# Optimization experiments

Measured on AMD Instinct MI355X. Metric: run time of the kernel, lower is better.

## Reference

```python
import jax, jax.numpy as jnp
import numpy as np

GROUP_SIZE = 64
NUM_HEADS = 16
NUM_KV_HEADS = 4
ROPE_BASE = 10000.0


def rms_norm(x):
    eps = jnp.asarray(jnp.finfo(x.dtype).eps, x.dtype)
    return x * jax.lax.rsqrt(jnp.mean(x * x, axis=-1, keepdims=True) + eps)


def ternary_weight(w, g=GROUP_SIZE):
    # fake-quant with straight-through estimator, matching torch bf16 cast
    wb = w.astype(jnp.bfloat16)
    wg = wb.reshape(-1, g)
    scale = jnp.clip(jnp.mean(jnp.abs(wg), axis=-1, keepdims=True), 1e-8)
    q = jnp.clip(jnp.round(wg / scale), -1, 1)
    wq = (q * scale).reshape(w.shape)
    return wb + jax.lax.stop_gradient(wq - wb)


def ternary_linear(x, w):
    wt = ternary_weight(w).astype(x.dtype)
    return x @ wt.T


def apply_rotary_emb(x, cos, sin):
    half = x.shape[-1] // 2
    x1, x2 = x[..., :half], x[..., half:]
    return jnp.concatenate((x1 * cos + x2 * sin, x1 * -sin + x2 * cos), axis=-1)


def rotary_tables(seq_len, head_dim, dtype):
    inv_freq = 1.0 / (ROPE_BASE ** (jnp.arange(0, head_dim, 2, dtype=jnp.float32) / head_dim))
    freqs = jnp.outer(jnp.arange(seq_len, dtype=jnp.float32), inv_freq)  # [S, D/2]
    cos = jnp.cos(freqs)[None, :, None, :].astype(dtype)  # [1,S,1,D/2]
    sin = jnp.sin(freqs)[None, :, None, :].astype(dtype)
    return cos, sin


def setup_inputs() -> dict:
    key = jax.random.key(0)
    k1, k2, k3 = jax.random.split(key, 3)
    dim = 1024
    q_size = NUM_HEADS * (dim // NUM_HEADS)
    kv_size = NUM_KV_HEADS * (dim // NUM_HEADS)
    return {
        "x": jax.random.normal(k1, (2, 2048, dim), dtype=jnp.float32),
        "w_qkv": jax.random.normal(k2, (q_size + 2 * kv_size, dim), dtype=jnp.float32) * 0.02,
        "w_proj": jax.random.normal(k3, (dim, dim), dtype=jnp.float32) * 0.02,
        "q_gain": jnp.ones((NUM_HEADS,), dtype=jnp.float32),
    }


def reference(x, w_qkv, w_proj, q_gain):
    bsz, seqlen, dim = x.shape
    head_dim = dim // NUM_HEADS
    q_size = NUM_HEADS * head_dim
    kv_size = NUM_KV_HEADS * head_dim

    qkv = ternary_linear(x, w_qkv)
    q = qkv[..., :q_size].reshape(bsz, seqlen, NUM_HEADS, head_dim)
    k = qkv[..., q_size:q_size + kv_size].reshape(bsz, seqlen, NUM_KV_HEADS, head_dim)
    v = qkv[..., q_size + kv_size:].reshape(bsz, seqlen, NUM_KV_HEADS, head_dim)

    q, k = rms_norm(q), rms_norm(k)
    cos, sin = rotary_tables(seqlen, head_dim, q.dtype)
    q = apply_rotary_emb(q, cos, sin)
    k = apply_rotary_emb(k, cos, sin)
    q = q * q_gain.astype(q.dtype)[None, None, :, None]

    # GQA: repeat kv heads
    rep = NUM_HEADS // NUM_KV_HEADS
    kr = jnp.repeat(k, rep, axis=2)  # [B,S,H,D]
    vr = jnp.repeat(v, rep, axis=2)

    scale = 1.0 / jnp.sqrt(jnp.asarray(head_dim, q.dtype))
    scores = jnp.einsum('bqhd,bkhd->bhqk', q, kr) * scale  # [B,H,S,S]
    causal = jnp.tril(jnp.ones((seqlen, seqlen), dtype=bool))
    scores = jnp.where(causal[None, None], scores, jnp.asarray(-jnp.inf, scores.dtype))
    probs = jax.nn.softmax(scores, axis=-1)
    y = jnp.einsum('bhqk,bkhd->bqhd', probs, vr).reshape(bsz, seqlen, dim)

    # NormedTernaryLinear: rms_norm then ternary linear
    return ternary_linear(rms_norm(y), w_proj)
```

## Files before the change

kernel.cpp:

```cpp
#include <hip/hip_runtime.h>
#include <cstdint>

typedef unsigned short u16;
typedef __bf16 bf16x8 __attribute__((ext_vector_type(8)));
typedef short s16x4 __attribute__((ext_vector_type(4)));
typedef int s32x2 __attribute__((ext_vector_type(2)));
typedef float f32x4 __attribute__((ext_vector_type(4)));

__device__ __forceinline__ u16 f2bf(float f) {
    unsigned u = __float_as_uint(f);
    u = (u + 0x7fffu + ((u >> 16) & 1u)) >> 16;
    return (u16)u;
}
__device__ __forceinline__ float bf2f(u16 h) {
    return __uint_as_float(((unsigned)h) << 16);
}

__device__ __forceinline__ void glds16(const u16* g, u16* l) {
    __builtin_amdgcn_global_load_lds(
        (const __attribute__((address_space(1))) void*)g,
        (__attribute__((address_space(3))) void*)l, 16, 0, 0);
}

__device__ __forceinline__ s16x4 pack_bf4(float p0, float p1, float p2, float p3) {
    unsigned a0 = __float_as_uint(p0) + 0x8000u;
    unsigned a1 = __float_as_uint(p1) + 0x8000u;
    unsigned a2 = __float_as_uint(p2) + 0x8000u;
    unsigned a3 = __float_as_uint(p3) + 0x8000u;
    s32x2 pk = {(int)__builtin_amdgcn_perm(a1, a0, 0x07060302u),
                (int)__builtin_amdgcn_perm(a3, a2, 0x07060302u)};
    return __builtin_bit_cast(s16x4, pk);
}

#if __has_builtin(__builtin_amdgcn_mfma_f32_16x16x16bf16_1k)
#define MFMA16(a, b, c) __builtin_amdgcn_mfma_f32_16x16x16bf16_1k(a, b, c, 0, 0, 0)
#else
static __device__ __forceinline__ f32x4 mfma16_asm(s16x4 a, s16x4 b, f32x4 c) {
    asm("v_mfma_f32_16x16x16_bf16 %0, %1, %2, %0" : "+v"(c) : "v"(a), "v"(b));
    return c;
}
#define MFMA16(a, b, c) mfma16_asm(a, b, c)
#endif

__global__ __launch_bounds__(256) void prep(
    const float* __restrict__ w_qkv, const float* __restrict__ w_proj,
    const float* __restrict__ x,
    u16* __restrict__ wqkv_b, u16* __restrict__ wproj_b, u16* __restrict__ xb) {
    int bid = blockIdx.x;
    if (bid < 1280) {
        const float* w; u16* o; size_t base;
        if (bid < 768) { w = w_qkv; o = wqkv_b; base = (size_t)bid * 2048; }
        else { w = w_proj; o = wproj_b; base = (size_t)(bid - 768) * 2048; }
        size_t i = base + (size_t)threadIdx.x * 8;
        float4 A = *(const float4*)(w + i);
        float4 B = *(const float4*)(w + i + 4);
        float wf[8] = {A.x, A.y, A.z, A.w, B.x, B.y, B.z, B.w};
        float wbf[8], ab[8];
        #pragma unroll
        for (int e = 0; e < 8; ++e) { wbf[e] = bf2f(f2bf(wf[e])); ab[e] = fabsf(wbf[e]); }
        float s = ((ab[0] + ab[1]) + (ab[2] + ab[3])) + ((ab[4] + ab[5]) + (ab[6] + ab[7]));
        s += __shfl_xor(s, 1);
        s += __shfl_xor(s, 2);
        s += __shfl_xor(s, 4);
        float scale = bf2f(f2bf(s * (1.0f / 64.0f)));
        if (scale < 1e-8f) scale = 1e-8f;
        u16 ov[8];
        #pragma unroll
        for (int e = 0; e < 8; ++e) {
            float t = bf2f(f2bf(wbf[e] / scale));
            float q = rintf(t);
            q = fminf(1.0f, fmaxf(-1.0f, q));
            float d = bf2f(f2bf(q * scale - wbf[e]));
            ov[e] = f2bf(wbf[e] + d);
        }
        *(int4*)(o + i) = *(const int4*)ov;
    } else {
        size_t i = ((size_t)(bid - 1280) * 256 + threadIdx.x) * 8;
        float4 a = *(const float4*)(x + i);
        float4 b = *(const float4*)(x + i + 4);
        u16 o[8] = {f2bf(a.x), f2bf(a.y), f2bf(a.z), f2bf(a.w),
                    f2bf(b.x), f2bf(b.y), f2bf(b.z), f2bf(b.w)};
        *(int4*)(xb + i) = *(const int4*)o;
    }
}

__global__ __launch_bounds__(256) void gemm_qkv(
    const u16* __restrict__ A, const u16* __restrict__ B,
    const float* __restrict__ gain,
    u16* __restrict__ Qb, u16* __restrict__ Kb, u16* __restrict__ Vt) {
    __shared__ u16 As[2][256 * 32];
    __shared__ u16 Bs[2][64 * 32];
    const int tid = threadIdx.x;
    const int lane = tid & 63, w = tid >> 6;
    const int quad = lane >> 4, l16 = lane & 15;
    const int bx = blockIdx.x, by = blockIdx.y;
    const int n0 = bx * 64, t0 = by * 256;
    const bool vblk = bx >= 20;
    const int K = 1024, nk = 32;
    const int b = by >> 3;

    const int sra = w * 16 + (lane >> 2);
    const int srb = tid >> 2;
    const int sg4 = lane & 3;

    f32x4 acc[4][4];
    f32x4 zero = {0.f, 0.f, 0.f, 0.f};
    #pragma unroll
    for (int i = 0; i < 4; ++i)
        #pragma unroll
        for (int j = 0; j < 4; ++j) acc[i][j] = zero;

    int aoff[4], boff[4];
    #pragma unroll
    for (int mi = 0; mi < 4; ++mi) {
        int r = w * 64 + mi * 16 + l16;
        aoff[mi] = r * 32 + (quad ^ ((r >> 1) & 3)) * 8;
    }
    #pragma unroll
    for (int ni = 0; ni < 4; ++ni) {
        int rb = ni * 16 + l16;
        boff[ni] = rb * 32 + (quad ^ ((rb >> 1) & 3)) * 8;
    }

    #pragma unroll
    for (int i = 0; i < 4; ++i) {
        int r = sra + i * 64;
        int g = sg4 ^ ((r >> 1) & 3);
        glds16(A + (size_t)(t0 + r) * K + g * 8, &As[0][0] + (w * 16 + i * 64) * 32 + lane * 8);
    }
    {
        int g = sg4 ^ ((srb >> 1) & 3);
        glds16(B + (size_t)(n0 + srb) * K + g * 8, &Bs[0][0] + w * 512 + lane * 8);
    }
    __syncthreads();

    for (int kt = 0; kt < nk; ++kt) {
        if (kt + 1 < nk) {
            int k0 = (kt + 1) * 32, bi = (kt + 1) & 1;
            #pragma unroll
            for (int i = 0; i < 4; ++i) {
                int r = sra + i * 64;
                int g = sg4 ^ ((r >> 1) & 3);
                glds16(A + (size_t)(t0 + r) * K + k0 + g * 8, &As[bi][0] + (w * 16 + i * 64) * 32 + lane * 8);
            }
            int g = sg4 ^ ((srb >> 1) & 3);
            glds16(B + (size_t)(n0 + srb) * K + k0 + g * 8, &Bs[bi][0] + w * 512 + lane * 8);
        }
        const u16* as = &As[kt & 1][0];
        const u16* bs = &Bs[kt & 1][0];
        bf16x8 af[4], bfr[4];
        #pragma unroll
        for (int mi = 0; mi < 4; ++mi) af[mi]  = *(const bf16x8*)(as + aoff[mi]);
        #pragma unroll
        for (int ni = 0; ni < 4; ++ni) bfr[ni] = *(const bf16x8*)(bs + boff[ni]);
        if (!vblk) {
            #pragma unroll
            for (int mi = 0; mi < 4; ++mi)
                #pragma unroll
                for (int ni = 0; ni < 4; ++ni)
                    acc[mi][ni] = __builtin_amdgcn_mfma_f32_16x16x32_bf16(af[mi], bfr[ni], acc[mi][ni], 0, 0, 0);
        } else {
            #pragma unroll
            for (int mi = 0; mi < 4; ++mi)
                #pragma unroll
                for (int ni = 0; ni < 4; ++ni)
                    acc[mi][ni] = __builtin_amdgcn_mfma_f32_16x16x32_bf16(bfr[ni], af[mi], acc[mi][ni], 0, 0, 0);
        }
        __syncthreads();
    }

    if (vblk) {
        const int kv = bx - 20;
        u16* vbase = Vt + (size_t)(b * 4 + kv) * 64 * 2048;
        const int si = (t0 + w * 64 + l16) & 2047;
        #pragma unroll
        for (int mi = 0; mi < 4; ++mi)
            #pragma unroll
            for (int ni = 0; ni < 4; ++ni) {
                int d = ni * 16 + quad * 4;
                #pragma unroll
                for (int r = 0; r < 4; ++r)
                    vbase[(size_t)(d + r) * 2048 + si + mi * 16] = f2bf(acc[mi][ni][r]);
            }
    } else {
        const bool isQ = bx < 16;
        const float sc = 0.18033688011112042f;
        const float g = isQ ? gain[bx] * sc : 1.0f;
        u16* base = isQ ? (Qb + (size_t)(b * 16 + bx) * 2048 * 64)
                        : (Kb + (size_t)(b * 4 + (bx - 16)) * 2048 * 64);
        const float eps = 1.1920929e-7f;
        const float invf0 = (float)(1.0 / pow(10000.0, (double)l16 / 32.0));
        const float invf1 = (float)(1.0 / pow(10000.0, (double)(l16 + 16) / 32.0));
        #pragma unroll
        for (int mi = 0; mi < 4; ++mi) {
            #pragma unroll
            for (int r = 0; r < 4; ++r) {
                float v0 = acc[mi][0][r], v1 = acc[mi][1][r];
                float v2 = acc[mi][2][r], v3 = acc[mi][3][r];
                float ssq = (v0 * v0 + v1 * v1) + (v2 * v2 + v3 * v3);
                #pragma unroll
                for (int m = 1; m < 16; m <<= 1) ssq += __shfl_xor(ssq, m);
                float rn = 1.0f / sqrtf(ssq * (1.0f / 64.0f) + eps);
                int si = (t0 + w * 64 + mi * 16 + quad * 4 + r) & 2047;
                float a0 = (float)si * invf0, a1 = (float)si * invf1;
                float c0 = __cosf(a0), s0 = __sinf(a0);
                float c1 = __cosf(a1), s1 = __sinf(a1);
                float x1a = v0 * rn, x2a = v2 * rn;
                float x1b = v1 * rn, x2b = v3 * rn;
                u16* row = base + (size_t)si * 64;
                row[l16]      = f2bf((x1a * c0 + x2a * s0) * g);
                row[l16 + 32] = f2bf((x2a * c0 - x1a * s0) * g);
                row[l16 + 16] = f2bf((x1b * c1 + x2b * s1) * g);
                row[l16 + 48] = f2bf((x2b * c1 - x1b * s1) * g);
            }
        }
    }
}

__global__ __launch_bounds__(256) void gemm_bt(
    const u16* __restrict__ A, const u16* __restrict__ B,
    float* __restrict__ C, int M, int N, int K) {
    __shared__ u16 As[2][128 * 32];
    __shared__ u16 Bs[2][64 * 32];
    const int tid = threadIdx.x;
    const int lane = tid & 63, w = tid >> 6;
    const int quad = lane >> 4, l16 = lane & 15;
    const int m0 = blockIdx.y * 128, n0 = blockIdx.x * 64;
    const int wm = (w >> 1) * 64, wn = (w & 1) * 32;

    const int sra = w * 16 + (lane >> 2);
    const int srb = tid >> 2;
    const int sg4 = lane & 3;

    f32x4 acc[4][2];
    f32x4 zero = {0.f, 0.f, 0.f, 0.f};
    #pragma unroll
    for (int i = 0; i < 4; ++i) { acc[i][0] = zero; acc[i][1] = zero; }

    int aoff[4], boff[2];
    #pragma unroll
    for (int mi = 0; mi < 4; ++mi) {
        int r = wm + mi * 16 + l16;
        aoff[mi] = r * 32 + (quad ^ ((r >> 1) & 3)) * 8;
    }
    #pragma unroll
    for (int ni = 0; ni < 2; ++ni) {
        int r = wn + ni * 16 + l16;
        boff[ni] = r * 32 + (quad ^ ((r >> 1) & 3)) * 8;
    }

    const int nk = K >> 5;
    #pragma unroll
    for (int i = 0; i < 2; ++i) {
        int r = sra + i * 64;
        int g = sg4 ^ ((r >> 1) & 3);
        glds16(A + (size_t)(m0 + r) * K + g * 8, &As[0][0] + (w * 16 + i * 64) * 32 + lane * 8);
    }
    {
        int g = sg4 ^ ((srb >> 1) & 3);
        glds16(B + (size_t)(n0 + srb) * K + g * 8, &Bs[0][0] + w * 512 + lane * 8);
    }
    __syncthreads();

    for (int kt = 0; kt < nk; ++kt) {
        if (kt + 1 < nk) {
            int k0 = (kt + 1) * 32, bi = (kt + 1) & 1;
            #pragma unroll
            for (int i = 0; i < 2; ++i) {
                int r = sra + i * 64;
                int g = sg4 ^ ((r >> 1) & 3);
                glds16(A + (size_t)(m0 + r) * K + k0 + g * 8, &As[bi][0] + (w * 16 + i * 64) * 32 + lane * 8);
            }
            int g = sg4 ^ ((srb >> 1) & 3);
            glds16(B + (size_t)(n0 + srb) * K + k0 + g * 8, &Bs[bi][0] + w * 512 + lane * 8);
        }
        const u16* as = &As[kt & 1][0];
        const u16* bs = &Bs[kt & 1][0];
        bf16x8 af[4], bfr[2];
        #pragma unroll
        for (int mi = 0; mi < 4; ++mi) af[mi]  = *(const bf16x8*)(as + aoff[mi]);
        #pragma unroll
        for (int ni = 0; ni < 2; ++ni) bfr[ni] = *(const bf16x8*)(bs + boff[ni]);
        #pragma unroll
        for (int mi = 0; mi < 4; ++mi)
            #pragma unroll
            for (int ni = 0; ni < 2; ++ni)
                acc[mi][ni] = __builtin_amdgcn_mfma_f32_16x16x32_bf16(af[mi], bfr[ni], acc[mi][ni], 0, 0, 0);
        __syncthreads();
    }
    #pragma unroll
    for (int mi = 0; mi < 4; ++mi)
        #pragma unroll
        for (int ni = 0; ni < 2; ++ni) {
            int rg = m0 + wm + mi * 16 + quad * 4;
            int cg = n0 + wn + ni * 16 + l16;
            float* cp = C + (size_t)rg * N + cg;
            #pragma unroll
            for (int r = 0; r < 4; ++r) cp[(size_t)r * N] = acc[mi][ni][r];
        }
}

__global__ __launch_bounds__(512, 4) void attn(
    const u16* __restrict__ Qb, const u16* __restrict__ Kb,
    const u16* __restrict__ Vt, const float* __restrict__ gain,
    float* __restrict__ y, float* __restrict__ Opart, float* __restrict__ ml) {
    __shared__ u16 Ks[2][64 * 64];
    __shared__ u16 Vsh[2][64 * 64];
    const int hb = blockIdx.x;
    const int h = hb & 15, b = hb >> 4, kvh = h >> 2;
    const int yid = blockIdx.y;
    int bq, c0; bool partial;
    if (yid < 16) { bq = 15 - (yid >> 1); c0 = (yid & 1) * 16; partial = true; }
    else          { bq = 23 - yid;        c0 = 0;              partial = false; }
    const int nj = partial ? (c0 ? (2 * bq - 14) : 16) : (2 * bq + 2);
    const int q0 = bq * 128;
    const int tid = threadIdx.x, lane = tid & 63, w = tid >> 6;
    const int quad = lane >> 4, l16 = lane & 15;
    const float nM = -(12.0f * fabsf(gain[h]) + 1.0f);

    const u16* Qg = Qb + ((size_t)(b * 16 + h) * 2048 + q0) * 64;
    const u16* Kg = Kb + (size_t)(b * 4 + kvh) * 2048 * 64;
    const u16* Vg = Vt + (size_t)(b * 4 + kvh) * 64 * 2048;

    const bf16x8 qa0 = *(const bf16x8*)(Qg + (size_t)(w * 16 + l16) * 64 + quad * 8);
    const bf16x8 qa1 = *(const bf16x8*)(Qg + (size_t)(w * 16 + l16) * 64 + 32 + quad * 8);

    const int sr = tid >> 3;
    const int sg = (tid & 7) ^ (sr & 7);
    u16* kd[2] = {&Ks[0][0] + tid * 8, &Ks[1][0] + tid * 8};
    u16* vd[2] = {&Vsh[0][0] + tid * 8, &Vsh[1][0] + tid * 8};

    {
        int c = (c0 + nj - 1) * 64;
        glds16(Kg + (size_t)(c + sr) * 64 + sg * 8, kd[(nj - 1) & 1]);
        glds16(Vg + (size_t)sr * 2048 + c + sg * 8, vd[(nj - 1) & 1]);
    }
    __syncthreads();

    f32x4 o[4];
    f32x4 zero = {0.f, 0.f, 0.f, 0.f};
    #pragma unroll
    for (int t = 0; t < 4; ++t) o[t] = zero;
    float l = 0.f;

    for (int jj = nj - 1; jj >= 0; --jj) {
        if (jj > 0) {
            int c = (c0 + jj - 1) * 64;
            glds16(Kg + (size_t)(c + sr) * 64 + sg * 8, kd[(jj - 1) & 1]);
            glds16(Vg + (size_t)sr * 2048 + c + sg * 8, vd[(jj - 1) & 1]);
        }
        const u16* Kt = (jj & 1) ? &Ks[1][0] : &Ks[0][0];
        const u16* Vl = (jj & 1) ? &Vsh[1][0] : &Vsh[0][0];
        const int d = 8 * bq + w - 4 * (c0 + jj);
        if (d >= 0) {
            const int tmax = d < 3 ? d : 3;
            f32x4 st[4];
            #pragma unroll
            for (int t = 0; t < 4; ++t) {
                if (t <= tmax) {
                    int rk = t * 16 + l16;
                    bf16x8 kb0 = *(const bf16x8*)(Kt + rk * 64 + ((quad ^ (rk & 7)) * 8));
                    bf16x8 kb1 = *(const bf16x8*)(Kt + rk * 64 + (((quad + 4) ^ (rk & 7)) * 8));
                    f32x4 s = __builtin_amdgcn_mfma_f32_16x16x32_bf16(kb0, qa0, zero, 0, 0, 0);
                    s = __builtin_amdgcn_mfma_f32_16x16x32_bf16(kb1, qa1, s, 0, 0, 0);
                    if (t == d) {
                        #pragma unroll
                        for (int r = 0; r < 4; ++r)
                            if (quad * 4 + r > l16) s[r] = -1e30f;
                    }
                    st[t] = s;
                }
            }
            float rs = 0.f;
            s16x4 pf[4];
            #pragma unroll
            for (int t = 0; t < 4; ++t) {
                if (t <= tmax) {
                    float p0 = __builtin_amdgcn_exp2f(st[t][0] + nM);
                    float p1 = __builtin_amdgcn_exp2f(st[t][1] + nM);
                    float p2 = __builtin_amdgcn_exp2f(st[t][2] + nM);
                    float p3 = __builtin_amdgcn_exp2f(st[t][3] + nM);
                    rs += (p0 + p1) + (p2 + p3);
                    pf[t] = pack_bf4(p0, p1, p2, p3);
                }
            }
            rs += __shfl_xor(rs, 16);
            rs += __shfl_xor(rs, 32);
            l += rs;
            #pragma unroll
            for (int dt = 0; dt < 4; ++dt) {
                int rv = dt * 16 + l16;
                #pragma unroll
                for (int kt = 0; kt < 4; ++kt) {
                    if (kt <= tmax) {
                        int gv = 2 * kt + (quad >> 1);
                        s16x4 va = *(const s16x4*)(Vl + rv * 64 + ((gv ^ (rv & 7)) * 8) + (quad & 1) * 4);
                        o[dt] = MFMA16(va, pf[kt], o[dt]);
                    }
                }
            }
        }
        __syncthreads();
    }

    const int q = w * 16 + l16;
    if (!partial) {
        const float inv = 1.0f / l;
        const size_t row = (size_t)b * 2048 + q0 + q;
        #pragma unroll
        for (int dt = 0; dt < 4; ++dt) {
            f32x4 a = o[dt] * inv;
            *(f32x4*)(&y[row * 1024 + h * 64 + dt * 16 + quad * 4]) = a;
        }
    } else {
        const int slot = (hb * 8 + (bq - 8)) * 2 + (c0 ? 1 : 0);
        float* Op = Opart + (size_t)slot * 8192;
        #pragma unroll
        for (int dt = 0; dt < 4; ++dt)
            *(f32x4*)(Op + q * 64 + dt * 16 + quad * 4) = o[dt];
        if (quad == 0) ml[slot * 128 + q] = l;
    }
}

__global__ __launch_bounds__(256) void rmsnorm_merge(
    const float* __restrict__ y, const float* __restrict__ Opart,
    const float* __restrict__ ml, u16* __restrict__ yb) {
    __shared__ float red[4];
    const int row = blockIdx.x, tid = threadIdx.x;
    const int b = row >> 11, s = row & 2047;
    float4 v;
    if (s < 1024) {
        v = *(const float4*)(y + (size_t)row * 1024 + tid * 4);
    } else {
        const int bq = s >> 7, q = s & 127;
        const int e = tid * 4, h = e >> 6, dh = e & 63;
        const int slot = ((b * 16 + h) * 8 + (bq - 8)) * 2;
        float l0 = ml[slot * 128 + q];
        float l1 = ml[(slot + 1) * 128 + q];
        float inv = 1.0f / (l0 + l1);
        const float* P0 = Opart + (size_t)slot * 8192 + q * 64 + dh;
        f32x4 x0 = *(const f32x4*)P0;
        f32x4 x1 = *(const f32x4*)(P0 + 8192);
        f32x4 r = (x0 + x1) * inv;
        v.x = r[0]; v.y = r[1]; v.z = r[2]; v.w = r[3];
    }
    float ss = v.x * v.x + v.y * v.y + v.z * v.z + v.w * v.w;
    #pragma unroll
    for (int m = 1; m < 64; m <<= 1) ss += __shfl_xor(ss, m);
    if ((tid & 63) == 0) red[tid >> 6] = ss;
    __syncthreads();
    float tot = red[0] + red[1] + red[2] + red[3];
    float rn = 1.0f / sqrtf(tot * (1.0f / 1024.0f) + 1.1920929e-7f);
    u16 o[4] = {f2bf(v.x * rn), f2bf(v.y * rn), f2bf(v.z * rn), f2bf(v.w * rn)};
    *(uint2*)(yb + (size_t)row * 1024 + tid * 4) = *(const uint2*)o;
}

extern "C" void kernel_launch(void* const* d_in, const int* in_sizes, int n_in,
                              void* d_out, int out_size, void* d_ws, size_t ws_size,
                              hipStream_t stream) {
    const float* x      = (const float*)d_in[0];
    const float* w_qkv  = (const float*)d_in[1];
    const float* w_proj = (const float*)d_in[2];
    const float* q_gain = (const float*)d_in[3];
    float* out = (float*)d_out;
    char* ws = (char*)d_ws;

    u16*   wproj_b = (u16*)(ws);
    u16*   xb      = (u16*)(ws + 2097152);
    float* y       = (float*)(ws + 2097152);
    u16*   wqkv_b  = (u16*)(ws + 10485760);
    u16*   Qb      = (u16*)(ws + 18874368);
    u16*   yb      = (u16*)(ws + 18874368);
    u16*   Kb      = (u16*)(ws + 27262976);
    u16*   Vt      = (u16*)(ws + 29360128);
    float* Opart   = (float*)(ws + 31457280);
    float* mlb     = (float*)(ws + 48234496);

    prep<<<3328, 256, 0, stream>>>(w_qkv, w_proj, x, wqkv_b, wproj_b, xb);
    gemm_qkv<<<dim3(24, 16), 256, 0, stream>>>(xb, wqkv_b, q_gain, Qb, Kb, Vt);
    attn<<<dim3(32, 24), 512, 0, stream>>>(Qb, Kb, Vt, q_gain, y, Opart, mlb);
    rmsnorm_merge<<<4096, 256, 0, stream>>>(y, Opart, mlb, yb);
    gemm_bt<<<dim3(16, 32), 256, 0, stream>>>(yb, wproj_b, out, 4096, 1024, 1024);
}
```

Baseline: 188.7 us.

## Rebalance attention split-K, shrink QKV GEMM tile, fold max offset into MFMA init

The QKV GEMM M-tile drops from 256 to 128 rows, doubling the grid so more CUs have work. The attention split-K scheme changes: query blocks 5-10 are split into two chunks and blocks 11-15 into three, giving 32 y-blocks per head instead of 24, and the merge kernel now sums two or three partial slots. The fixed max offset nM is folded into the MFMA accumulator init, the row-sum shuffle reduction is deferred to after the loop, s_setprio is raised around the MFMA sections, and bf16 packing uses native conversion. The cost is more partial-output traffic and a larger workspace footprint.

```diff
diff --git a/kernel.cpp b/kernel.cpp
--- a/kernel.cpp
+++ b/kernel.cpp
@@ -3,6 +3,7 @@
 
 typedef unsigned short u16;
 typedef __bf16 bf16x8 __attribute__((ext_vector_type(8)));
+typedef __bf16 bf16x2 __attribute__((ext_vector_type(2)));
 typedef short s16x4 __attribute__((ext_vector_type(4)));
 typedef int s32x2 __attribute__((ext_vector_type(2)));
 typedef float f32x4 __attribute__((ext_vector_type(4)));
@@ -23,12 +24,9 @@
 }
 
 __device__ __forceinline__ s16x4 pack_bf4(float p0, float p1, float p2, float p3) {
-    unsigned a0 = __float_as_uint(p0) + 0x8000u;
-    unsigned a1 = __float_as_uint(p1) + 0x8000u;
-    unsigned a2 = __float_as_uint(p2) + 0x8000u;
-    unsigned a3 = __float_as_uint(p3) + 0x8000u;
-    s32x2 pk = {(int)__builtin_amdgcn_perm(a1, a0, 0x07060302u),
-                (int)__builtin_amdgcn_perm(a3, a2, 0x07060302u)};
+    bf16x2 lo = {(__bf16)p0, (__bf16)p1};
+    bf16x2 hi = {(__bf16)p2, (__bf16)p3};
+    s32x2 pk = {__builtin_bit_cast(int, lo), __builtin_bit_cast(int, hi)};
     return __builtin_bit_cast(s16x4, pk);
 }
 
@@ -88,32 +86,32 @@
     const u16* __restrict__ A, const u16* __restrict__ B,
     const float* __restrict__ gain,
     u16* __restrict__ Qb, u16* __restrict__ Kb, u16* __restrict__ Vt) {
-    __shared__ u16 As[2][256 * 32];
+    __shared__ u16 As[2][128 * 32];
     __shared__ u16 Bs[2][64 * 32];
     const int tid = threadIdx.x;
     const int lane = tid & 63, w = tid >> 6;
     const int quad = lane >> 4, l16 = lane & 15;
     const int bx = blockIdx.x, by = blockIdx.y;
-    const int n0 = bx * 64, t0 = by * 256;
+    const int n0 = bx * 64, t0 = by * 128;
     const bool vblk = bx >= 20;
     const int K = 1024, nk = 32;
-    const int b = by >> 3;
+    const int b = by >> 4;
 
     const int sra = w * 16 + (lane >> 2);
     const int srb = tid >> 2;
     const int sg4 = lane & 3;
 
-    f32x4 acc[4][4];
+    f32x4 acc[2][4];
     f32x4 zero = {0.f, 0.f, 0.f, 0.f};
     #pragma unroll
-    for (int i = 0; i < 4; ++i)
+    for (int i = 0; i < 2; ++i)
         #pragma unroll
         for (int j = 0; j < 4; ++j) acc[i][j] = zero;
 
-    int aoff[4], boff[4];
-    #pragma unroll
-    for (int mi = 0; mi < 4; ++mi) {
-        int r = w * 64 + mi * 16 + l16;
+    int aoff[2], boff[4];
+    #pragma unroll
+    for (int mi = 0; mi < 2; ++mi) {
+        int r = w * 32 + mi * 16 + l16;
         aoff[mi] = r * 32 + (quad ^ ((r >> 1) & 3)) * 8;
     }
     #pragma unroll
@@ -123,7 +121,7 @@
     }
 
     #pragma unroll
-    for (int i = 0; i < 4; ++i) {
+    for (int i = 0; i < 2; ++i) {
         int r = sra + i * 64;
         int g = sg4 ^ ((r >> 1) & 3);
         glds16(A + (size_t)(t0 + r) * K + g * 8, &As[0][0] + (w * 16 + i * 64) * 32 + lane * 8);
@@ -138,7 +136,7 @@
         if (kt + 1 < nk) {
             int k0 = (kt + 1) * 32, bi = (kt + 1) & 1;
             #pragma unroll
-            for (int i = 0; i < 4; ++i) {
+            for (int i = 0; i < 2; ++i) {
                 int r = sra + i * 64;
                 int g = sg4 ^ ((r >> 1) & 3);
                 glds16(A + (size_t)(t0 + r) * K + k0 + g * 8, &As[bi][0] + (w * 16 + i * 64) * 32 + lane * 8);
@@ -148,20 +146,20 @@
         }
         const u16* as = &As[kt & 1][0];
         const u16* bs = &Bs[kt & 1][0];
-        bf16x8 af[4], bfr[4];
-        #pragma unroll
-        for (int mi = 0; mi < 4; ++mi) af[mi]  = *(const bf16x8*)(as + aoff[mi]);
+        bf16x8 af[2], bfr[4];
+        #pragma unroll
+        for (int mi = 0; mi < 2; ++mi) af[mi]  = *(const bf16x8*)(as + aoff[mi]);
         #pragma unroll
         for (int ni = 0; ni < 4; ++ni) bfr[ni] = *(const bf16x8*)(bs + boff[ni]);
         if (!vblk) {
             #pragma unroll
-            for (int mi = 0; mi < 4; ++mi)
+            for (int mi = 0; mi < 2; ++mi)
                 #pragma unroll
                 for (int ni = 0; ni < 4; ++ni)
                     acc[mi][ni] = __builtin_amdgcn_mfma_f32_16x16x32_bf16(af[mi], bfr[ni], acc[mi][ni], 0, 0, 0);
         } else {
             #pragma unroll
-            for (int mi = 0; mi < 4; ++mi)
+            for (int mi = 0; mi < 2; ++mi)
                 #pragma unroll
                 for (int ni = 0; ni < 4; ++ni)
                     acc[mi][ni] = __builtin_amdgcn_mfma_f32_16x16x32_bf16(bfr[ni], af[mi], acc[mi][ni], 0, 0, 0);
@@ -172,9 +170,9 @@
     if (vblk) {
         const int kv = bx - 20;
         u16* vbase = Vt + (size_t)(b * 4 + kv) * 64 * 2048;
-        const int si = (t0 + w * 64 + l16) & 2047;
-        #pragma unroll
-        for (int mi = 0; mi < 4; ++mi)
+        const int si = (t0 + w * 32 + l16) & 2047;
+        #pragma unroll
+        for (int mi = 0; mi < 2; ++mi)
             #pragma unroll
             for (int ni = 0; ni < 4; ++ni) {
                 int d = ni * 16 + quad * 4;
@@ -192,7 +190,7 @@
         const float invf0 = (float)(1.0 / pow(10000.0, (double)l16 / 32.0));
         const float invf1 = (float)(1.0 / pow(10000.0, (double)(l16 + 16) / 32.0));
         #pragma unroll
-        for (int mi = 0; mi < 4; ++mi) {
+        for (int mi = 0; mi < 2; ++mi) {
             #pragma unroll
             for (int r = 0; r < 4; ++r) {
                 float v0 = acc[mi][0][r], v1 = acc[mi][1][r];
@@ -201,7 +199,7 @@
                 #pragma unroll
                 for (int m = 1; m < 16; m <<= 1) ssq += __shfl_xor(ssq, m);
                 float rn = 1.0f / sqrtf(ssq * (1.0f / 64.0f) + eps);
-                int si = (t0 + w * 64 + mi * 16 + quad * 4 + r) & 2047;
+                int si = (t0 + w * 32 + mi * 16 + quad * 4 + r) & 2047;
                 float a0 = (float)si * invf0, a1 = (float)si * invf1;
                 float c0 = __cosf(a0), s0 = __sinf(a0);
                 float c1 = __cosf(a1), s1 = __sinf(a1);
@@ -309,14 +307,23 @@
     const int hb = blockIdx.x;
     const int h = hb & 15, b = hb >> 4, kvh = h >> 2;
     const int yid = blockIdx.y;
-    int bq, c0; bool partial;
-    if (yid < 16) { bq = 15 - (yid >> 1); c0 = (yid & 1) * 16; partial = true; }
-    else          { bq = 23 - yid;        c0 = 0;              partial = false; }
-    const int nj = partial ? (c0 ? (2 * bq - 14) : 16) : (2 * bq + 2);
+    int bq, c0, nj, sb = 0; bool partial;
+    if (yid < 5) {
+        bq = yid; c0 = 0; nj = 2 * bq + 2; partial = false;
+    } else if (yid < 17) {
+        int t = yid - 5; bq = 5 + (t >> 1); int ch = t & 1, T = 2 * bq + 2;
+        c0 = (ch * T) >> 1; nj = (((ch + 1) * T) >> 1) - c0; partial = true;
+        sb = (bq - 5) * 2 + ch;
+    } else {
+        int t = yid - 17; bq = 11 + t / 3; int ch = t - (t / 3) * 3, T = 2 * bq + 2;
+        c0 = ch * T / 3; nj = (ch + 1) * T / 3 - c0; partial = true;
+        sb = 12 + (bq - 11) * 3 + ch;
+    }
     const int q0 = bq * 128;
     const int tid = threadIdx.x, lane = tid & 63, w = tid >> 6;
     const int quad = lane >> 4, l16 = lane & 15;
     const float nM = -(12.0f * fabsf(gain[h]) + 1.0f);
+    const f32x4 minit = {nM, nM, nM, nM};
 
     const u16* Qg = Qb + ((size_t)(b * 16 + h) * 2048 + q0) * 64;
     const u16* Kg = Kb + (size_t)(b * 4 + kvh) * 2048 * 64;
@@ -355,13 +362,14 @@
         if (d >= 0) {
             const int tmax = d < 3 ? d : 3;
             f32x4 st[4];
+            __builtin_amdgcn_s_setprio(1);
             #pragma unroll
             for (int t = 0; t < 4; ++t) {
                 if (t <= tmax) {
                     int rk = t * 16 + l16;
                     bf16x8 kb0 = *(const bf16x8*)(Kt + rk * 64 + ((quad ^ (rk & 7)) * 8));
                     bf16x8 kb1 = *(const bf16x8*)(Kt + rk * 64 + (((quad + 4) ^ (rk & 7)) * 8));
-                    f32x4 s = __builtin_amdgcn_mfma_f32_16x16x32_bf16(kb0, qa0, zero, 0, 0, 0);
+                    f32x4 s = __builtin_amdgcn_mfma_f32_16x16x32_bf16(kb0, qa0, minit, 0, 0, 0);
                     s = __builtin_amdgcn_mfma_f32_16x16x32_bf16(kb1, qa1, s, 0, 0, 0);
                     if (t == d) {
                         #pragma unroll
@@ -371,22 +379,22 @@
                     st[t] = s;
                 }
             }
+            __builtin_amdgcn_s_setprio(0);
             float rs = 0.f;
             s16x4 pf[4];
             #pragma unroll
             for (int t = 0; t < 4; ++t) {
                 if (t <= tmax) {
-                    float p0 = __builtin_amdgcn_exp2f(st[t][0] + nM);
-                    float p1 = __builtin_amdgcn_exp2f(st[t][1] + nM);
-                    float p2 = __builtin_amdgcn_exp2f(st[t][2] + nM);
-                    float p3 = __builtin_amdgcn_exp2f(st[t][3] + nM);
+                    float p0 = __builtin_amdgcn_exp2f(st[t][0]);
+                    float p1 = __builtin_amdgcn_exp2f(st[t][1]);
+                    float p2 = __builtin_amdgcn_exp2f(st[t][2]);
+                    float p3 = __builtin_amdgcn_exp2f(st[t][3]);
                     rs += (p0 + p1) + (p2 + p3);
                     pf[t] = pack_bf4(p0, p1, p2, p3);
                 }
             }
-            rs += __shfl_xor(rs, 16);
-            rs += __shfl_xor(rs, 32);
             l += rs;
+            __builtin_amdgcn_s_setprio(1);
             #pragma unroll
             for (int dt = 0; dt < 4; ++dt) {
                 int rv = dt * 16 + l16;
@@ -399,9 +407,13 @@
                     }
                 }
             }
+            __builtin_amdgcn_s_setprio(0);
         }
         __syncthreads();
     }
+
+    l += __shfl_xor(l, 16);
+    l += __shfl_xor(l, 32);
 
     const int q = w * 16 + l16;
     if (!partial) {
@@ -413,7 +425,7 @@
             *(f32x4*)(&y[row * 1024 + h * 64 + dt * 16 + quad * 4]) = a;
         }
     } else {
-        const int slot = (hb * 8 + (bq - 8)) * 2 + (c0 ? 1 : 0);
+        const int slot = hb * 27 + sb;
         float* Op = Opart + (size_t)slot * 8192;
         #pragma unroll
         for (int dt = 0; dt < 4; ++dt)
@@ -429,20 +441,23 @@
     const int row = blockIdx.x, tid = threadIdx.x;
     const int b = row >> 11, s = row & 2047;
     float4 v;
-    if (s < 1024) {
+    if (s < 640) {
         v = *(const float4*)(y + (size_t)row * 1024 + tid * 4);
     } else {
         const int bq = s >> 7, q = s & 127;
         const int e = tid * 4, h = e >> 6, dh = e & 63;
-        const int slot = ((b * 16 + h) * 8 + (bq - 8)) * 2;
-        float l0 = ml[slot * 128 + q];
-        float l1 = ml[(slot + 1) * 128 + q];
-        float inv = 1.0f / (l0 + l1);
+        const int ns = bq < 11 ? 2 : 3;
+        const int sb = bq < 11 ? (bq - 5) * 2 : 12 + (bq - 11) * 3;
+        const int slot = (b * 16 + h) * 27 + sb;
+        float l = ml[slot * 128 + q] + ml[(slot + 1) * 128 + q];
         const float* P0 = Opart + (size_t)slot * 8192 + q * 64 + dh;
-        f32x4 x0 = *(const f32x4*)P0;
-        f32x4 x1 = *(const f32x4*)(P0 + 8192);
-        f32x4 r = (x0 + x1) * inv;
-        v.x = r[0]; v.y = r[1]; v.z = r[2]; v.w = r[3];
+        f32x4 x = *(const f32x4*)P0 + *(const f32x4*)(P0 + 8192);
+        if (ns == 3) {
+            l += ml[(slot + 2) * 128 + q];
+            x += *(const f32x4*)(P0 + 16384);
+        }
+        float inv = 1.0f / l;
+        v.x = x[0] * inv; v.y = x[1] * inv; v.z = x[2] * inv; v.w = x[3] * inv;
     }
     float ss = v.x * v.x + v.y * v.y + v.z * v.z + v.w * v.w;
     #pragma unroll
@@ -474,11 +489,11 @@
     u16*   Kb      = (u16*)(ws + 27262976);
     u16*   Vt      = (u16*)(ws + 29360128);
     float* Opart   = (float*)(ws + 31457280);
-    float* mlb     = (float*)(ws + 48234496);
+    float* mlb     = (float*)(ws + 59768832);
 
     prep<<<3328, 256, 0, stream>>>(w_qkv, w_proj, x, wqkv_b, wproj_b, xb);
-    gemm_qkv<<<dim3(24, 16), 256, 0, stream>>>(xb, wqkv_b, q_gain, Qb, Kb, Vt);
-    attn<<<dim3(32, 24), 512, 0, stream>>>(Qb, Kb, Vt, q_gain, y, Opart, mlb);
+    gemm_qkv<<<dim3(24, 32), 256, 0, stream>>>(xb, wqkv_b, q_gain, Qb, Kb, Vt);
+    attn<<<dim3(32, 32), 512, 0, stream>>>(Qb, Kb, Vt, q_gain, y, Opart, mlb);
     rmsnorm_merge<<<4096, 256, 0, stream>>>(y, Opart, mlb, yb);
     gemm_bt<<<dim3(16, 32), 256, 0, stream>>>(yb, wproj_b, out, 4096, 1024, 1024);
 }
```

New measurement: 181.5 us. 1.04x faster.
